# Kernel tuning notes

Hardware: AMD Instinct MI355X
Metric: run time of the kernel (lower is better)

Reference implementation:

```python
import jax, jax.numpy as jnp
import numpy as np

B, C_IN, T, N = 16, 64, 12, 1024
KS, C_OUT = 3, 64


def setup_inputs() -> dict:
    key = jax.random.key(0)
    k1, k2, k3 = jax.random.split(key, 3)
    x = jax.random.normal(k1, (B, C_IN, T, N), dtype=jnp.float32)
    # graph Chebyshev kernel [N, Ks*N]; scale down so matmuls stay well-conditioned
    kernel = jax.random.normal(k2, (N, KS * N), dtype=jnp.float32) / np.sqrt(N)
    # xavier-uniform theta [Ks*c_in, c_out]
    limit = np.sqrt(6.0 / (KS * C_IN + C_OUT))
    theta = jax.random.uniform(k3, (KS * C_IN, C_OUT), dtype=jnp.float32,
                               minval=-limit, maxval=limit)
    bias = jnp.zeros((C_OUT,), dtype=jnp.float32)
    return {"x": x, "kernel": kernel, "theta": theta, "bias": bias}


def reference(x, kernel, theta, bias):
    # x: [B, C, T, N]; kernel: [N, Ks*N] viewed as [N, Ks, N]; theta: [C*Ks, c_out]
    Bb, C, Tt, Nn = x.shape
    Ks = kernel.shape[1] // Nn
    Kr = kernel.reshape(Nn, Ks, Nn)            # [n, k, m]
    th = theta.reshape(C, Ks, -1)              # [c, k, o] (row index = c*Ks + k)
    # batched spectral conv over all timesteps at once (fuses the per-t loop)
    x_mul = jnp.einsum('bctn,nkm->bctkm', x, Kr)       # [B,C,T,Ks,N]
    gc = jnp.einsum('bctkm,cko->botm', x_mul, th)      # [B,c_out,T,N]
    gc = gc + bias[None, :, None, None]
    # c_in == c_out -> residual is identity
    return jax.nn.relu(gc + x)
```

## Files before the change

kernel.cpp:

```cpp
#include <hip/hip_runtime.h>

#define NB   16
#define NC   64
#define NT   12
#define NN   1024
#define NKS  3

typedef float  f32x4  __attribute__((ext_vector_type(4)));
typedef short  s16x8  __attribute__((ext_vector_type(8)));
typedef unsigned short u16x4 __attribute__((ext_vector_type(4)));
typedef unsigned short u16x8 __attribute__((ext_vector_type(8)));
typedef unsigned short ush;

__device__ __forceinline__ ush f2bf(float f) {
    union { float f; unsigned u; } v; v.f = f;
    unsigned r = v.u + 0x7FFFu + ((v.u >> 16) & 1u);
    return (ush)(r >> 16);
}

__device__ __forceinline__ void cp16(const void* g, void* l) {
    __builtin_amdgcn_global_load_lds(
        (const __attribute__((address_space(1))) unsigned int*)g,
        (__attribute__((address_space(3))) unsigned int*)l, 16, 0, 0);
}

#define APAN_OFF 0
#define KB_OFF   25165824
#define TH_OFF   31457280

__global__ __launch_bounds__(256)
void spatio_prep(const float* __restrict__ x, const float* __restrict__ kern,
                 const float* __restrict__ theta,
                 ush* __restrict__ apan, ush* __restrict__ kb, ush* __restrict__ thbf)
{
    const int blk = blockIdx.x;
    const int tid = threadIdx.x;

    if (blk < 1536) {
        int ch   = blk * 256 + tid;
        int rest = ch / 1536;
        int c    = ch - rest * 1536;
        int kt   = rest & 15, mtp = rest >> 4;
        int j    = c >> 3, pp = c & 7;
        int d    = pp ^ (j & 7);
        int k    = j >> 6, mm = j & 63;
        int col  = (k << 10) + (mtp << 6) + mm;
        int n0   = (kt << 6) + (d << 3);
        u16x8 w;
#pragma unroll
        for (int i = 0; i < 8; ++i)
            w[i] = f2bf(kern[(size_t)(n0 + i) * (NKS * NN) + col]);
        ((u16x8*)kb)[ch] = w;
    } else if (blk < 1584) {
        int id = (blk - 1536) * 256 + tid;
        if (id < 12288) {
            int row = id >> 6, o = id & 63;
            int cc = row / 3, k = row - 3 * cc;
            thbf[o * 192 + k * 64 + cc] = f2bf(theta[id]);
        }
    } else {
        int id  = (blk - 1584) * 256 + tid;
        int c   = id & 2047;
        int kt  = (id >> 11) & 15;
        int g4  = id >> 15;
        int row = c >> 3, pp = c & 7;
        int d   = pp ^ (row & 7);
        int bl  = row >> 6, cc = row & 63;
        int bt  = g4 * 4 + bl;
        int b   = bt / NT, t = bt - NT * b;
        const float* src = x + ((size_t)((b * NC + cc) * NT + t)) * NN + (kt << 6) + (d << 3);
        float4 a0 = ((const float4*)src)[0];
        float4 a1 = ((const float4*)src)[1];
        u16x8 w;
        w[0] = f2bf(a0.x); w[1] = f2bf(a0.y); w[2] = f2bf(a0.z); w[3] = f2bf(a0.w);
        w[4] = f2bf(a1.x); w[5] = f2bf(a1.y); w[6] = f2bf(a1.z); w[7] = f2bf(a1.w);
        ((u16x8*)apan)[id] = w;
    }
}

__global__ __launch_bounds__(512, 1)
void spatio_main(const ush* __restrict__ apan, const ush* __restrict__ kb,
                 const ush* __restrict__ thbf, const float* __restrict__ bias,
                 const float* __restrict__ x, float* __restrict__ out)
{
    __shared__ __attribute__((aligned(128))) char smem[114688];

    const int tid  = threadIdx.x;
    const int bid  = blockIdx.x;
    const int wg   = (bid & 7) * 96 + (bid >> 3);
    const int g4   = wg >> 4;
    const int mt   = wg & 15;
    const int lane = tid & 63;
    const int wid  = tid >> 6;
    const int wr   = wid >> 1;
    const int wn   = wid & 1;
    const int quad = lane >> 4;
    const int l16  = lane & 15;
    const int swz  = l16 & 7;

    const char* abase = (const char*)apan + ((size_t)g4 << 19);
    const char* bbase = (const char*)kb   + ((size_t)mt * 393216);

    f32x4 acc[4][6];
#pragma unroll
    for (int i = 0; i < 4; ++i)
#pragma unroll
        for (int j = 0; j < 6; ++j) acc[i][j] = (f32x4){0.f, 0.f, 0.f, 0.f};

#define STAGE(tt, pp) do {                                                  \
        const char* as_ = abase + ((size_t)(tt) << 15);                     \
        const char* bs_ = bbase + (size_t)(tt) * 24576;                     \
        char* la_ = smem + (pp) * 57344;                                    \
        char* lb_ = la_ + 32768;                                            \
        _Pragma("unroll")                                                   \
        for (int i_ = 0; i_ < 4; ++i_)                                      \
            cp16(as_ + (i_ * 512 + tid) * 16, la_ + (i_ * 512 + tid) * 16); \
        _Pragma("unroll")                                                   \
        for (int i_ = 0; i_ < 3; ++i_)                                      \
            cp16(bs_ + (i_ * 512 + tid) * 16, lb_ + (i_ * 512 + tid) * 16); \
    } while (0)

    STAGE(0, 0);
    STAGE(1, 1);
    asm volatile("s_waitcnt vmcnt(7)" ::: "memory");
    __builtin_amdgcn_s_barrier();
    asm volatile("" ::: "memory");

#pragma unroll 2
    for (int t = 0; t < 16; ++t) {
        const int p = t & 1;
        const ush (*As)[64] = (const ush (*)[64])(smem + p * 57344);
        const ush (*Bs)[64] = (const ush (*)[64])(smem + p * 57344 + 32768);
        s16x8 af[4];
#pragma unroll
        for (int kk = 0; kk < 2; ++kk)
#pragma unroll
            for (int g = 0; g < 2; ++g) {
                if (g == 0) {
#pragma unroll
                    for (int rb = 0; rb < 4; ++rb)
                        af[rb] = *(const s16x8*)&As[64 * wr + 16 * rb + l16]
                                                  [((kk * 4 + quad) ^ swz) << 3];
                }
                s16x8 bf[3];
#pragma unroll
                for (int jj = 0; jj < 3; ++jj)
                    bf[jj] = *(const s16x8*)&Bs[96 * wn + 48 * g + 16 * jj + l16]
                                               [((kk * 4 + quad) ^ swz) << 3];
                __builtin_amdgcn_s_setprio(1);
#pragma unroll
                for (int rb = 0; rb < 4; ++rb)
#pragma unroll
                    for (int jj = 0; jj < 3; ++jj)
                        acc[rb][3 * g + jj] = __builtin_amdgcn_mfma_f32_16x16x32_bf16(
                            af[rb], bf[jj], acc[rb][3 * g + jj], 0, 0, 0);
                __builtin_amdgcn_s_setprio(0);
                if (!(kk == 1 && g == 1)) {
                    asm volatile("" ::: "memory");
                    __builtin_amdgcn_s_barrier();
                    asm volatile("" ::: "memory");
                }
            }
        asm volatile("s_waitcnt lgkmcnt(0)" ::: "memory");
        __builtin_amdgcn_s_barrier();
        asm volatile("" ::: "memory");
        if (t < 14) {
            STAGE(t + 2, p);
            asm volatile("s_waitcnt vmcnt(7)" ::: "memory");
            __builtin_amdgcn_s_barrier();
            asm volatile("" ::: "memory");
        } else if (t == 14) {
            asm volatile("s_waitcnt vmcnt(0)" ::: "memory");
            __builtin_amdgcn_s_barrier();
            asm volatile("" ::: "memory");
        }
    }
#undef STAGE

    ush (*xm)[64][200] = (ush (*)[64][200])smem;
#pragma unroll
    for (int rb = 0; rb < 4; ++rb)
#pragma unroll
        for (int jb = 0; jb < 6; ++jb) {
            int J   = 96 * wn + 16 * jb + l16;
            int kk2 = J >> 6, mm = J & 63;
            int ck0 = (kk2 << 6) + 16 * rb + (quad << 2);
            u16x4 w;
            w.x = f2bf(acc[rb][jb].x); w.y = f2bf(acc[rb][jb].y);
            w.z = f2bf(acc[rb][jb].z); w.w = f2bf(acc[rb][jb].w);
            *(u16x4*)&xm[wr][mm][ck0] = w;
        }
    __syncthreads();

    const int bt2 = wid & 3, hh = wid >> 2;
    f32x4 acc2[4][2];
#pragma unroll
    for (int i = 0; i < 4; ++i) {
        acc2[i][0] = (f32x4){0.f, 0.f, 0.f, 0.f};
        acc2[i][1] = (f32x4){0.f, 0.f, 0.f, 0.f};
    }
#pragma unroll
    for (int ks = 0; ks < 6; ++ks) {
        s16x8 b2[2];
#pragma unroll
        for (int jm = 0; jm < 2; ++jm)
            b2[jm] = *(const s16x8*)&xm[bt2][(hh << 5) + (jm << 4) + l16]
                                            [(ks << 5) + (quad << 3)];
#pragma unroll
        for (int of = 0; of < 4; ++of) {
            s16x8 a2 = *(const s16x8*)(thbf + (size_t)((of << 4) + l16) * 192
                                            + (ks << 5) + (quad << 3));
#pragma unroll
            for (int jm = 0; jm < 2; ++jm)
                acc2[of][jm] = __builtin_amdgcn_mfma_f32_16x16x32_bf16(
                    a2, b2[jm], acc2[of][jm], 0, 0, 0);
        }
    }

    const int bt = (g4 << 2) + bt2;
    const int b  = bt / NT, tt = bt - NT * b;
#pragma unroll
    for (int of = 0; of < 4; ++of)
#pragma unroll
        for (int jm = 0; jm < 2; ++jm) {
            int mm = (hh << 5) + (jm << 4) + l16;
#pragma unroll
            for (int r = 0; r < 4; ++r) {
                int o = (of << 4) + (quad << 2) + r;
                size_t idx = ((size_t)((b * NC + o) * NT + tt)) * NN + (mt << 6) + mm;
                float v = acc2[of][jm][r] + bias[o] + x[idx];
                out[idx] = fmaxf(v, 0.f);
            }
        }
}

extern "C" void kernel_launch(void* const* d_in, const int* in_sizes, int n_in,
                              void* d_out, int out_size, void* d_ws, size_t ws_size,
                              hipStream_t stream) {
    const float* x     = (const float*)d_in[0];
    const float* kern  = (const float*)d_in[1];
    const float* theta = (const float*)d_in[2];
    const float* bias  = (const float*)d_in[3];
    float* out = (float*)d_out;
    (void)in_sizes; (void)n_in; (void)out_size; (void)ws_size;

    ush* apan = (ush*)((char*)d_ws + APAN_OFF);
    ush* kbp  = (ush*)((char*)d_ws + KB_OFF);
    ush* thbf = (ush*)((char*)d_ws + TH_OFF);

    hipLaunchKernelGGL(spatio_prep, dim3(7728), dim3(256), 0, stream,
                       x, kern, theta, apan, kbp, thbf);
    hipLaunchKernelGGL(spatio_main, dim3(768), dim3(512), 0, stream,
                       apan, kbp, thbf, bias, x, out);
}
```

Baseline: 206.0 us.

## Restructure GEMM main loop into 4-stage K=32 ring with vectorized kernel prep

The main GEMM now loads 32-wide K slices into a four-slot shared-memory ring with three stages in flight, with one barrier per iteration instead of several. The bf16 panels get a new swizzle to match. The prep kernel now reads the graph kernel with float4 row loads instead of strided scalar loads. Launch bounds allow two blocks per CU, and the grid becomes 2D with no block remapping. This trades L2-friendly block ordering and deeper per-stage MFMA work for less synchronization and better load overlap. Occupancy of 2 cannot actually be reached given the 112KB shared memory per block.

Measured after the change: 210.5 us. +2.2%, slower.

```diff
diff --git a/kernel.cpp b/kernel.cpp
--- a/kernel.cpp
+++ b/kernel.cpp
@@ -36,49 +36,58 @@
     const int blk = blockIdx.x;
     const int tid = threadIdx.x;
 
-    if (blk < 1536) {
-        int ch   = blk * 256 + tid;
-        int rest = ch / 1536;
-        int c    = ch - rest * 1536;
-        int kt   = rest & 15, mtp = rest >> 4;
-        int j    = c >> 3, pp = c & 7;
-        int d    = pp ^ (j & 7);
-        int k    = j >> 6, mm = j & 63;
-        int col  = (k << 10) + (mtp << 6) + mm;
-        int n0   = (kt << 6) + (d << 3);
-        u16x8 w;
-#pragma unroll
-        for (int i = 0; i < 8; ++i)
-            w[i] = f2bf(kern[(size_t)(n0 + i) * (NKS * NN) + col]);
-        ((u16x8*)kb)[ch] = w;
-    } else if (blk < 1584) {
-        int id = (blk - 1536) * 256 + tid;
-        if (id < 12288) {
-            int row = id >> 6, o = id & 63;
-            int cc = row / 3, k = row - 3 * cc;
-            thbf[o * 192 + k * 64 + cc] = f2bf(theta[id]);
-        }
-    } else {
-        int id  = (blk - 1584) * 256 + tid;
-        int c   = id & 2047;
-        int kt  = (id >> 11) & 15;
+    if (blk < 6144) {
+        int id  = blk * 256 + tid;
+        int c   = id & 1023;
+        int sub = (id >> 10) & 31;
         int g4  = id >> 15;
-        int row = c >> 3, pp = c & 7;
-        int d   = pp ^ (row & 7);
-        int bl  = row >> 6, cc = row & 63;
-        int bt  = g4 * 4 + bl;
+        int r   = c >> 2, p = c & 3;
+        int d   = p ^ (r & 3);
+        int bl  = r >> 6, ch = r & 63;
+        int bt  = 4 * g4 + bl;
         int b   = bt / NT, t = bt - NT * b;
-        const float* src = x + ((size_t)((b * NC + cc) * NT + t)) * NN + (kt << 6) + (d << 3);
+        const float* src = x + ((size_t)((b * NC + ch) * NT + t)) * NN + sub * 32 + d * 8;
         float4 a0 = ((const float4*)src)[0];
         float4 a1 = ((const float4*)src)[1];
         u16x8 w;
         w[0] = f2bf(a0.x); w[1] = f2bf(a0.y); w[2] = f2bf(a0.z); w[3] = f2bf(a0.w);
         w[4] = f2bf(a1.x); w[5] = f2bf(a1.y); w[6] = f2bf(a1.z); w[7] = f2bf(a1.w);
         ((u16x8*)apan)[id] = w;
-    }
-}
-
-__global__ __launch_bounds__(512, 1)
+    } else if (blk < 6528) {
+        int id  = (blk - 6144) * 256 + tid;
+        int d   = id & 3;
+        int jq  = (id >> 2) % 48;
+        int r2  = (id >> 2) / 48;
+        int sub = r2 & 31;
+        int mt  = r2 >> 5;
+        int j0  = jq * 4;
+        int colbase = ((j0 >> 6) << 10) + (mt << 6) + (j0 & 63);
+        int n0  = sub * 32 + d * 8;
+        float4 v[8];
+#pragma unroll
+        for (int i = 0; i < 8; ++i)
+            v[i] = *(const float4*)&kern[(size_t)(n0 + i) * (NKS * NN) + colbase];
+        int cbase = (mt * 32 + sub) * 768;
+#pragma unroll
+        for (int jj = 0; jj < 4; ++jj) {
+            u16x8 w;
+            w[0] = f2bf(v[0][jj]); w[1] = f2bf(v[1][jj]);
+            w[2] = f2bf(v[2][jj]); w[3] = f2bf(v[3][jj]);
+            w[4] = f2bf(v[4][jj]); w[5] = f2bf(v[5][jj]);
+            w[6] = f2bf(v[6][jj]); w[7] = f2bf(v[7][jj]);
+            ((u16x8*)kb)[cbase + (j0 + jj) * 4 + (d ^ jj)] = w;
+        }
+    } else {
+        int id = (blk - 6528) * 256 + tid;
+        if (id < 12288) {
+            int row = id >> 6, o = id & 63;
+            int c = row / 3, k = row - 3 * c;
+            thbf[o * 192 + k * 64 + c] = f2bf(theta[id]);
+        }
+    }
+}
+
+__global__ __launch_bounds__(512, 2)
 void spatio_main(const ush* __restrict__ apan, const ush* __restrict__ kb,
                  const ush* __restrict__ thbf, const float* __restrict__ bias,
                  const float* __restrict__ x, float* __restrict__ out)
@@ -86,20 +95,26 @@
     __shared__ __attribute__((aligned(128))) char smem[114688];
 
     const int tid  = threadIdx.x;
-    const int bid  = blockIdx.x;
-    const int wg   = (bid & 7) * 96 + (bid >> 3);
-    const int g4   = wg >> 4;
-    const int mt   = wg & 15;
+    const int g4   = blockIdx.x;
+    const int mt   = blockIdx.y;
     const int lane = tid & 63;
     const int wid  = tid >> 6;
     const int wr   = wid >> 1;
     const int wn   = wid & 1;
     const int quad = lane >> 4;
     const int l16  = lane & 15;
-    const int swz  = l16 & 7;
-
-    const char* abase = (const char*)apan + ((size_t)g4 << 19);
-    const char* bbase = (const char*)kb   + ((size_t)mt * 393216);
+    const int swz16 = (quad ^ (l16 & 3)) << 4;
+
+    const char* abase = (const char*)apan + (size_t)g4 * 524288;
+    const char* bbase = (const char*)kb   + (size_t)mt * 393216;
+
+    int aoff[4], boff[6];
+#pragma unroll
+    for (int rb = 0; rb < 4; ++rb)
+        aoff[rb] = (64 * wr + 16 * rb + l16) * 64 + swz16;
+#pragma unroll
+    for (int jb = 0; jb < 6; ++jb)
+        boff[jb] = 16384 + (96 * wn + 16 * jb + l16) * 64 + swz16;
 
     f32x4 acc[4][6];
 #pragma unroll
@@ -107,77 +122,51 @@
 #pragma unroll
         for (int j = 0; j < 6; ++j) acc[i][j] = (f32x4){0.f, 0.f, 0.f, 0.f};
 
-#define STAGE(tt, pp) do {                                                  \
-        const char* as_ = abase + ((size_t)(tt) << 15);                     \
-        const char* bs_ = bbase + (size_t)(tt) * 24576;                     \
-        char* la_ = smem + (pp) * 57344;                                    \
-        char* lb_ = la_ + 32768;                                            \
-        _Pragma("unroll")                                                   \
-        for (int i_ = 0; i_ < 4; ++i_)                                      \
-            cp16(as_ + (i_ * 512 + tid) * 16, la_ + (i_ * 512 + tid) * 16); \
-        _Pragma("unroll")                                                   \
-        for (int i_ = 0; i_ < 3; ++i_)                                      \
-            cp16(bs_ + (i_ * 512 + tid) * 16, lb_ + (i_ * 512 + tid) * 16); \
+#define STAGE(tt) do {                                                        \
+        const char* as_ = abase + (size_t)(tt) * 16384;                       \
+        const char* bs_ = bbase + (size_t)(tt) * 12288;                       \
+        char* sl_ = smem + ((tt) & 3) * 28672;                                \
+        if (tid < 448) {                                                      \
+            _Pragma("unroll")                                                 \
+            for (int i_ = 0; i_ < 4; ++i_) {                                  \
+                int c_ = i_ * 448 + tid;                                      \
+                const char* g_ = (c_ < 1024) ? (as_ + c_ * 16)                \
+                                             : (bs_ + (c_ - 1024) * 16);      \
+                cp16(g_, sl_ + c_ * 16);                                      \
+            }                                                                 \
+        }                                                                     \
     } while (0)
 
-    STAGE(0, 0);
-    STAGE(1, 1);
-    asm volatile("s_waitcnt vmcnt(7)" ::: "memory");
-    __builtin_amdgcn_s_barrier();
-    asm volatile("" ::: "memory");
-
-#pragma unroll 2
-    for (int t = 0; t < 16; ++t) {
-        const int p = t & 1;
-        const ush (*As)[64] = (const ush (*)[64])(smem + p * 57344);
-        const ush (*Bs)[64] = (const ush (*)[64])(smem + p * 57344 + 32768);
-        s16x8 af[4];
-#pragma unroll
-        for (int kk = 0; kk < 2; ++kk)
-#pragma unroll
-            for (int g = 0; g < 2; ++g) {
-                if (g == 0) {
-#pragma unroll
-                    for (int rb = 0; rb < 4; ++rb)
-                        af[rb] = *(const s16x8*)&As[64 * wr + 16 * rb + l16]
-                                                  [((kk * 4 + quad) ^ swz) << 3];
-                }
-                s16x8 bf[3];
-#pragma unroll
-                for (int jj = 0; jj < 3; ++jj)
-                    bf[jj] = *(const s16x8*)&Bs[96 * wn + 48 * g + 16 * jj + l16]
-                                               [((kk * 4 + quad) ^ swz) << 3];
-                __builtin_amdgcn_s_setprio(1);
-#pragma unroll
-                for (int rb = 0; rb < 4; ++rb)
-#pragma unroll
-                    for (int jj = 0; jj < 3; ++jj)
-                        acc[rb][3 * g + jj] = __builtin_amdgcn_mfma_f32_16x16x32_bf16(
-                            af[rb], bf[jj], acc[rb][3 * g + jj], 0, 0, 0);
-                __builtin_amdgcn_s_setprio(0);
-                if (!(kk == 1 && g == 1)) {
-                    asm volatile("" ::: "memory");
-                    __builtin_amdgcn_s_barrier();
-                    asm volatile("" ::: "memory");
-                }
-            }
-        asm volatile("s_waitcnt lgkmcnt(0)" ::: "memory");
+    STAGE(0); STAGE(1); STAGE(2);
+
+    for (int t = 0; t < 32; ++t) {
+        if (t < 30)       asm volatile("s_waitcnt vmcnt(8)" ::: "memory");
+        else if (t == 30) asm volatile("s_waitcnt vmcnt(4)" ::: "memory");
+        else              asm volatile("s_waitcnt vmcnt(0)" ::: "memory");
         __builtin_amdgcn_s_barrier();
         asm volatile("" ::: "memory");
-        if (t < 14) {
-            STAGE(t + 2, p);
-            asm volatile("s_waitcnt vmcnt(7)" ::: "memory");
-            __builtin_amdgcn_s_barrier();
-            asm volatile("" ::: "memory");
-        } else if (t == 14) {
-            asm volatile("s_waitcnt vmcnt(0)" ::: "memory");
-            __builtin_amdgcn_s_barrier();
-            asm volatile("" ::: "memory");
-        }
+        if (t + 3 < 32) STAGE(t + 3);
+        const char* sl = smem + (t & 3) * 28672;
+        s16x8 af[4], bf[6];
+#pragma unroll
+        for (int rb = 0; rb < 4; ++rb) af[rb] = *(const s16x8*)(sl + aoff[rb]);
+#pragma unroll
+        for (int jb = 0; jb < 6; ++jb) bf[jb] = *(const s16x8*)(sl + boff[jb]);
+        asm volatile("s_waitcnt lgkmcnt(0)" ::: "memory");
+        __builtin_amdgcn_sched_barrier(0);
+        __builtin_amdgcn_s_setprio(1);
+#pragma unroll
+        for (int rb = 0; rb < 4; ++rb)
+#pragma unroll
+            for (int jb = 0; jb < 6; ++jb)
+                acc[rb][jb] = __builtin_amdgcn_mfma_f32_16x16x32_bf16(
+                    af[rb], bf[jb], acc[rb][jb], 0, 0, 0);
+        __builtin_amdgcn_s_setprio(0);
     }
 #undef STAGE
 
     ush (*xm)[64][200] = (ush (*)[64][200])smem;
+    __syncthreads();
 #pragma unroll
     for (int rb = 0; rb < 4; ++rb)
 #pragma unroll
@@ -248,8 +237,8 @@
     ush* kbp  = (ush*)((char*)d_ws + KB_OFF);
     ush* thbf = (ush*)((char*)d_ws + TH_OFF);
 
-    hipLaunchKernelGGL(spatio_prep, dim3(7728), dim3(256), 0, stream,
+    hipLaunchKernelGGL(spatio_prep, dim3(6576), dim3(256), 0, stream,
                        x, kern, theta, apan, kbp, thbf);
-    hipLaunchKernelGGL(spatio_main, dim3(768), dim3(512), 0, stream,
+    hipLaunchKernelGGL(spatio_main, dim3(48, 16), dim3(512), 0, stream,
                        apan, kbp, thbf, bias, x, out);
 }
```
